# Optimization experiments

Hardware: AMD Instinct MI355X
Metric: run time of the kernel (lower is better)

## Reference

```python
import jax, jax.numpy as jnp
import numpy as np

LAMBDA_CONT = 0.01
SIGMA = 1.0


def _pairwise_dist(x):
    # Euclidean cdist(x, x): [N, N]
    sq = jnp.sum(x * x, axis=-1)  # [N]
    d2 = sq[:, None] + sq[None, :] - 2.0 * (x @ x.T)
    d2 = jnp.maximum(d2, 0.0)
    # safe sqrt (grad 0 at 0, matching torch.cdist subgradient)
    return jnp.where(d2 > 0, jnp.sqrt(jnp.where(d2 > 0, d2, 1.0)), 0.0)


def setup_inputs() -> dict:
    key = jax.random.key(0)
    k1, k2 = jax.random.split(key)
    points = jax.random.normal(k1, (8192, 2), dtype=jnp.float32)
    outputs = jax.random.uniform(k2, (8192, 8), dtype=jnp.float32)
    return {"points": points, "outputs": outputs}


def reference(points, outputs):
    n = points.shape[0]
    dist = _pairwise_dist(points)                     # [N, N]
    weights = jnp.exp(-(dist * dist) / (2.0 * SIGMA ** 2))
    weights = weights * (1.0 - jnp.eye(n, dtype=points.dtype))
    diff = _pairwise_dist(outputs)                    # [N, N]
    loss = jnp.sum(weights * diff) / (n * (n - 1))
    return LAMBDA_CONT * loss
```

## Files before the change

### kernel.cpp

```cpp
#include <hip/hip_runtime.h>


typedef float v2f __attribute__((ext_vector_type(2)));
typedef float v4f __attribute__((ext_vector_type(4)));
typedef _Float16 h4 __attribute__((ext_vector_type(4)));
typedef float f32x4 __attribute__((ext_vector_type(4)));

constexpr int N_PTS  = 8192;
constexpr int TDIM   = N_PTS / 64;
constexpr int NTILES = TDIM * (TDIM + 1) / 2;
constexpr int WPB    = 4;
constexpr int NBLOCKS = NTILES / WPB;

constexpr float KE = -0.72134752044448169f;
constexpr float M2 =  1.4426950408889634f;

__device__ __forceinline__ int tri_before(int r) {
    return r * TDIM - (r * (r - 1)) / 2;
}

__global__ __launch_bounds__(256, 4) void cont_pairs(
    const float* __restrict__ points, const float* __restrict__ outputs,
    double* __restrict__ partials)
{
    const int tid  = threadIdx.x;
    const int wid  = tid >> 6;
    const int lane = tid & 63;
    const int g    = blockIdx.x * WPB + wid;

    int ti = (int)((2 * TDIM + 1 -
                    sqrtf((float)((2 * TDIM + 1) * (2 * TDIM + 1) - 8 * g))) * 0.5f);
    ti = ti < 0 ? 0 : (ti > TDIM - 1 ? TDIM - 1 : ti);
    while (tri_before(ti + 1) <= g) ++ti;
    while (tri_before(ti) > g) --ti;
    const int tj = ti + (g - tri_before(ti));
    const bool diag = (ti == tj);

    const int q = lane >> 4, cl = lane & 15;
    const int rowbase = ti * 64, colbase = tj * 64;

    const _Float16 h0 = (_Float16)0.f, h1 = (_Float16)1.f;

    h4 aO[4], aP[4];
    #pragma unroll
    for (int it = 0; it < 4; ++it) {
        const int i = rowbase + it * 16 + cl;
        const v4f* o = reinterpret_cast<const v4f*>(outputs + 8 * i);
        const v4f x = o[0], y = o[1];
        const v4f s = x * x + y * y;
        const float on = (s.x + s.y) + (s.z + s.w);
        const v2f p = reinterpret_cast<const v2f*>(points)[i];
        const float pn = p.x * p.x + p.y * p.y;
        h4 a;
        if (q == 0)      a = h4{(_Float16)x.x, (_Float16)x.y, (_Float16)x.z, (_Float16)x.w};
        else if (q == 1) a = h4{(_Float16)y.x, (_Float16)y.y, (_Float16)y.z, (_Float16)y.w};
        else if (q == 2) a = h4{(_Float16)on, h1, h0, h0};
        else             a = h4{h0, h0, h0, h0};
        aO[it] = a;
        if (q == 0) aP[it] = h4{(_Float16)p.x, (_Float16)p.y, (_Float16)(KE * pn), h1};
        else        aP[it] = h4{h0, h0, h0, h0};
    }

    float accE[4] = {0.f, 0.f, 0.f, 0.f};

    v4f jx, jy; v2f jp;
    {
        const int j = colbase + cl;
        const v4f* o = reinterpret_cast<const v4f*>(outputs + 8 * j);
        jx = o[0]; jy = o[1];
        jp = reinterpret_cast<const v2f*>(points)[j];
    }

    #pragma unroll
    for (int jt = 0; jt < 4; ++jt) {
        const v4f s = jx * jx + jy * jy;
        const float on = (s.x + s.y) + (s.z + s.w);
        const float pn = jp.x * jp.x + jp.y * jp.y;
        h4 bO, bP;
        if (q == 0)      bO = h4{(_Float16)(-2.f * jx.x), (_Float16)(-2.f * jx.y),
                                 (_Float16)(-2.f * jx.z), (_Float16)(-2.f * jx.w)};
        else if (q == 1) bO = h4{(_Float16)(-2.f * jy.x), (_Float16)(-2.f * jy.y),
                                 (_Float16)(-2.f * jy.z), (_Float16)(-2.f * jy.w)};
        else if (q == 2) bO = h4{h1, (_Float16)on, h0, h0};
        else             bO = h4{h0, h0, h0, h0};
        if (q == 0) bP = h4{(_Float16)(M2 * jp.x), (_Float16)(M2 * jp.y), h1,
                            (_Float16)(KE * pn)};
        else        bP = h4{h0, h0, h0, h0};
        const int jcol = jt * 16 + cl;

        if (jt < 3) {
            const int jn = colbase + (jt + 1) * 16 + cl;
            const v4f* o = reinterpret_cast<const v4f*>(outputs + 8 * jn);
            jx = o[0]; jy = o[1];
            jp = reinterpret_cast<const v2f*>(points)[jn];
        }

        #pragma unroll
        for (int it = 0; it < 4; ++it) {
            const f32x4 z = {0.f, 0.f, 0.f, 0.f};
            f32x4 dO = __builtin_amdgcn_mfma_f32_16x16x16f16(aO[it], bO, z, 0, 0, 0);
            f32x4 dP = __builtin_amdgcn_mfma_f32_16x16x16f16(aP[it], bP, z, 0, 0, 0);
            #pragma unroll
            for (int e = 0; e < 4; ++e) {
                float diff = __builtin_amdgcn_sqrtf(fmaxf(dO[e], 0.f));
                if (diag) {
                    const int irow = it * 16 + q * 4 + e;
                    diff = (jcol > irow) ? diff : 0.f;
                }
                accE[e] = fmaf(__builtin_amdgcn_exp2f(dP[e]), diff, accE[e]);
            }
        }
    }

    float accS = (accE[0] + accE[1]) + (accE[2] + accE[3]);
    #pragma unroll
    for (int off = 32; off > 0; off >>= 1)
        accS += __shfl_down(accS, off, 64);

    __shared__ float wpart[WPB];
    if (lane == 0) wpart[wid] = accS;
    __syncthreads();
    if (tid == 0) {
        double d = 0.0;
        #pragma unroll
        for (int w = 0; w < WPB; ++w) d += (double)wpart[w];
        partials[blockIdx.x] = d;
    }
}

__global__ __launch_bounds__(256) void cont_final(
    const double* __restrict__ partials, int nparts,
    float* __restrict__ out, double scale)
{
    const int tid = threadIdx.x;
    double sum = 0.0;
    for (int i = tid; i < nparts; i += 256) sum += partials[i];
    #pragma unroll
    for (int off = 32; off > 0; off >>= 1)
        sum += __shfl_down(sum, off, 64);

    __shared__ double ws[256 / 64];
    if ((tid & 63) == 0) ws[tid >> 6] = sum;
    __syncthreads();
    if (tid == 0) {
        double t = 0.0;
        #pragma unroll
        for (int w = 0; w < 256 / 64; ++w) t += ws[w];
        out[0] = (float)(t * scale);
    }
}

extern "C" void kernel_launch(void* const* d_in, const int* in_sizes, int n_in,
                              void* d_out, int out_size, void* d_ws, size_t ws_size,
                              hipStream_t stream) {
    const float* points  = (const float*)d_in[0];
    const float* outputs = (const float*)d_in[1];
    float* out = (float*)d_out;

    const int n = in_sizes[0] / 2;
    double* partials = (double*)d_ws;

    cont_pairs<<<dim3(NBLOCKS), dim3(256), 0, stream>>>(points, outputs, partials);

    const double scale = 0.01 * 2.0 / ((double)n * (double)(n - 1));
    cont_final<<<1, 256, 0, stream>>>(partials, NBLOCKS, out, scale);
}
```

Measured before the change: 26.40 us.

## Precompute fp16 MFMA operand tables in a prep kernel

Adds a prep kernel that builds the fp16 A/B operand fragments for outputs and points once per 16-row tile and writes them to workspace. The pair kernel then loads ready-made h4 fragments with coalesced loads instead of recomputing norms and conversions for every tile it visits. The final reduction now runs with 1024 threads. This adds a third kernel launch and extra workspace traffic in exchange for less per-tile ALU work.

```diff
diff --git a/kernel.cpp b/kernel.cpp
--- a/kernel.cpp
+++ b/kernel.cpp
@@ -7,6 +7,7 @@
 typedef float f32x4 __attribute__((ext_vector_type(4)));
 
 constexpr int N_PTS  = 8192;
+constexpr int T16    = N_PTS / 16;
 constexpr int TDIM   = N_PTS / 64;
 constexpr int NTILES = TDIM * (TDIM + 1) / 2;
 constexpr int WPB    = 4;
@@ -19,8 +20,48 @@
     return r * TDIM - (r * (r - 1)) / 2;
 }
 
+__global__ __launch_bounds__(256) void cont_prep(
+    const float* __restrict__ points, const float* __restrict__ outputs,
+    h4* __restrict__ AO, h4* __restrict__ AP,
+    h4* __restrict__ BO, h4* __restrict__ BP)
+{
+    const int idx = blockIdx.x * 256 + threadIdx.x;
+    const int l  = idx & 63;
+    const int t  = idx >> 6;
+    const int q  = l >> 4, cl = l & 15;
+    const int row = t * 16 + cl;
+
+    const v4f* o = reinterpret_cast<const v4f*>(outputs + 8 * row);
+    const v4f x = o[0], y = o[1];
+    const v4f s = x * x + y * y;
+    const float on = (s.x + s.y) + (s.z + s.w);
+    const v2f p = reinterpret_cast<const v2f*>(points)[row];
+    const float pn = p.x * p.x + p.y * p.y;
+
+    const _Float16 h0 = (_Float16)0.f, h1 = (_Float16)1.f;
+    h4 ao, ap, bo, bp;
+    if (q == 0)      ao = h4{(_Float16)x.x, (_Float16)x.y, (_Float16)x.z, (_Float16)x.w};
+    else if (q == 1) ao = h4{(_Float16)y.x, (_Float16)y.y, (_Float16)y.z, (_Float16)y.w};
+    else if (q == 2) ao = h4{(_Float16)on, h1, h0, h0};
+    else             ao = h4{h0, h0, h0, h0};
+    if (q == 0) ap = h4{(_Float16)p.x, (_Float16)p.y, (_Float16)(KE * pn), h1};
+    else        ap = h4{h0, h0, h0, h0};
+    if (q == 0)      bo = h4{(_Float16)(-2.f * x.x), (_Float16)(-2.f * x.y),
+                             (_Float16)(-2.f * x.z), (_Float16)(-2.f * x.w)};
+    else if (q == 1) bo = h4{(_Float16)(-2.f * y.x), (_Float16)(-2.f * y.y),
+                             (_Float16)(-2.f * y.z), (_Float16)(-2.f * y.w)};
+    else if (q == 2) bo = h4{h1, (_Float16)on, h0, h0};
+    else             bo = h4{h0, h0, h0, h0};
+    if (q == 0) bp = h4{(_Float16)(M2 * p.x), (_Float16)(M2 * p.y), h1,
+                        (_Float16)(KE * pn)};
+    else        bp = h4{h0, h0, h0, h0};
+
+    AO[idx] = ao; AP[idx] = ap; BO[idx] = bo; BP[idx] = bp;
+}
+
 __global__ __launch_bounds__(256, 4) void cont_pairs(
-    const float* __restrict__ points, const float* __restrict__ outputs,
+    const h4* __restrict__ AO, const h4* __restrict__ AP,
+    const h4* __restrict__ BO, const h4* __restrict__ BP,
     double* __restrict__ partials)
 {
     const int tid  = threadIdx.x;
@@ -37,69 +78,26 @@
     const bool diag = (ti == tj);
 
     const int q = lane >> 4, cl = lane & 15;
-    const int rowbase = ti * 64, colbase = tj * 64;
 
-    const _Float16 h0 = (_Float16)0.f, h1 = (_Float16)1.f;
-
-    h4 aO[4], aP[4];
+    h4 aO[4], aP[4], bO[4], bP[4];
     #pragma unroll
     for (int it = 0; it < 4; ++it) {
-        const int i = rowbase + it * 16 + cl;
-        const v4f* o = reinterpret_cast<const v4f*>(outputs + 8 * i);
-        const v4f x = o[0], y = o[1];
-        const v4f s = x * x + y * y;
-        const float on = (s.x + s.y) + (s.z + s.w);
-        const v2f p = reinterpret_cast<const v2f*>(points)[i];
-        const float pn = p.x * p.x + p.y * p.y;
-        h4 a;
-        if (q == 0)      a = h4{(_Float16)x.x, (_Float16)x.y, (_Float16)x.z, (_Float16)x.w};
-        else if (q == 1) a = h4{(_Float16)y.x, (_Float16)y.y, (_Float16)y.z, (_Float16)y.w};
-        else if (q == 2) a = h4{(_Float16)on, h1, h0, h0};
-        else             a = h4{h0, h0, h0, h0};
-        aO[it] = a;
-        if (q == 0) aP[it] = h4{(_Float16)p.x, (_Float16)p.y, (_Float16)(KE * pn), h1};
-        else        aP[it] = h4{h0, h0, h0, h0};
+        const int ta = (ti * 4 + it) * 64 + lane;
+        aO[it] = AO[ta]; aP[it] = AP[ta];
+        const int tb = (tj * 4 + it) * 64 + lane;
+        bO[it] = BO[tb]; bP[it] = BP[tb];
     }
 
     float accE[4] = {0.f, 0.f, 0.f, 0.f};
 
-    v4f jx, jy; v2f jp;
-    {
-        const int j = colbase + cl;
-        const v4f* o = reinterpret_cast<const v4f*>(outputs + 8 * j);
-        jx = o[0]; jy = o[1];
-        jp = reinterpret_cast<const v2f*>(points)[j];
-    }
-
     #pragma unroll
     for (int jt = 0; jt < 4; ++jt) {
-        const v4f s = jx * jx + jy * jy;
-        const float on = (s.x + s.y) + (s.z + s.w);
-        const float pn = jp.x * jp.x + jp.y * jp.y;
-        h4 bO, bP;
-        if (q == 0)      bO = h4{(_Float16)(-2.f * jx.x), (_Float16)(-2.f * jx.y),
-                                 (_Float16)(-2.f * jx.z), (_Float16)(-2.f * jx.w)};
-        else if (q == 1) bO = h4{(_Float16)(-2.f * jy.x), (_Float16)(-2.f * jy.y),
-                                 (_Float16)(-2.f * jy.z), (_Float16)(-2.f * jy.w)};
-        else if (q == 2) bO = h4{h1, (_Float16)on, h0, h0};
-        else             bO = h4{h0, h0, h0, h0};
-        if (q == 0) bP = h4{(_Float16)(M2 * jp.x), (_Float16)(M2 * jp.y), h1,
-                            (_Float16)(KE * pn)};
-        else        bP = h4{h0, h0, h0, h0};
         const int jcol = jt * 16 + cl;
-
-        if (jt < 3) {
-            const int jn = colbase + (jt + 1) * 16 + cl;
-            const v4f* o = reinterpret_cast<const v4f*>(outputs + 8 * jn);
-            jx = o[0]; jy = o[1];
-            jp = reinterpret_cast<const v2f*>(points)[jn];
-        }
-
         #pragma unroll
         for (int it = 0; it < 4; ++it) {
             const f32x4 z = {0.f, 0.f, 0.f, 0.f};
-            f32x4 dO = __builtin_amdgcn_mfma_f32_16x16x16f16(aO[it], bO, z, 0, 0, 0);
-            f32x4 dP = __builtin_amdgcn_mfma_f32_16x16x16f16(aP[it], bP, z, 0, 0, 0);
+            f32x4 dO = __builtin_amdgcn_mfma_f32_16x16x16f16(aO[it], bO[jt], z, 0, 0, 0);
+            f32x4 dP = __builtin_amdgcn_mfma_f32_16x16x16f16(aP[it], bP[jt], z, 0, 0, 0);
             #pragma unroll
             for (int e = 0; e < 4; ++e) {
                 float diff = __builtin_amdgcn_sqrtf(fmaxf(dO[e], 0.f));
@@ -128,24 +126,24 @@
     }
 }
 
-__global__ __launch_bounds__(256) void cont_final(
+__global__ __launch_bounds__(1024) void cont_final(
     const double* __restrict__ partials, int nparts,
     float* __restrict__ out, double scale)
 {
     const int tid = threadIdx.x;
     double sum = 0.0;
-    for (int i = tid; i < nparts; i += 256) sum += partials[i];
+    for (int i = tid; i < nparts; i += 1024) sum += partials[i];
     #pragma unroll
     for (int off = 32; off > 0; off >>= 1)
         sum += __shfl_down(sum, off, 64);
 
-    __shared__ double ws[256 / 64];
+    __shared__ double ws[1024 / 64];
     if ((tid & 63) == 0) ws[tid >> 6] = sum;
     __syncthreads();
     if (tid == 0) {
         double t = 0.0;
         #pragma unroll
-        for (int w = 0; w < 256 / 64; ++w) t += ws[w];
+        for (int w = 0; w < 1024 / 64; ++w) t += ws[w];
         out[0] = (float)(t * scale);
     }
 }
@@ -158,10 +156,17 @@
     float* out = (float*)d_out;
 
     const int n = in_sizes[0] / 2;
-    double* partials = (double*)d_ws;
+    constexpr size_t TBL = (size_t)T16 * 64 * sizeof(h4);
+    h4* AO = (h4*)d_ws;
+    h4* AP = (h4*)((char*)d_ws + TBL);
+    h4* BO = (h4*)((char*)d_ws + 2 * TBL);
+    h4* BP = (h4*)((char*)d_ws + 3 * TBL);
+    double* partials = (double*)((char*)d_ws + 4 * TBL);
 
-    cont_pairs<<<dim3(NBLOCKS), dim3(256), 0, stream>>>(points, outputs, partials);
+    cont_prep<<<dim3(T16 * 64 / 256), dim3(256), 0, stream>>>(
+        points, outputs, AO, AP, BO, BP);
+    cont_pairs<<<dim3(NBLOCKS), dim3(256), 0, stream>>>(AO, AP, BO, BP, partials);
 
     const double scale = 0.01 * 2.0 / ((double)n * (double)(n - 1));
-    cont_final<<<1, 256, 0, stream>>>(partials, NBLOCKS, out, scale);
+    cont_final<<<1, 1024, 0, stream>>>(partials, NBLOCKS, out, scale);
 }
```

Result: faster. 23.19 us, median of 2 (-12.2%).
